# Optimization experiments

Measured on AMD Instinct MI355X. Metric: run time of the kernel, lower is better.

## Reference

```python
import jax, jax.numpy as jnp
import numpy as np

# Fixed hierarchical grouping of the 15 regions into 5 groups of 3 (from split_regions)
SPLIT_IDX = np.array([[0, 1, 8], [2, 4, 6], [3, 5, 7], [9, 11, 13], [10, 12, 14]])
BN_EPS = 1e-5


def _bn_relu(x, g, b):
    # BatchNorm over (batch, spatial) dims in training-stats mode, then ReLU
    mu = jnp.mean(x, axis=(0, 2, 3), keepdims=True)
    var = jnp.var(x, axis=(0, 2, 3), keepdims=True)
    xn = (x - mu) * jax.lax.rsqrt(var + BN_EPS)
    return jax.nn.relu(xn * g[None, :, None, None] + b[None, :, None, None])


def _local_agg(x, params):
    # x: [B, Cin, G, K]; pointwise conv (1x1) -> BN -> ReLU per layer, then max over K
    for W, g, b in params:
        x = jnp.einsum('oi,bigk->bogk', W, x)
        x = _bn_relu(x, g, b)
    return jnp.max(x, axis=-1)  # [B, Cout, G]


def setup_inputs() -> dict:
    key = jax.random.key(0)
    ks = jax.random.split(key, 8)
    B, G, K = 32, 15, 2048
    inp = {"local_regions": jax.random.normal(ks[0], (B, G, K, 3), jnp.float32)}
    chans = [(3, 64, 64), (67, 128, 128), (131, 256, 256)]
    ki = 1
    for li, (c0, c1, c2) in enumerate(chans):
        for wi, (co, ci) in enumerate([(c1, c0), (c2, c1)]):
            inp[f"la{li}_w{wi}"] = jax.random.normal(ks[ki], (co, ci), jnp.float32) * (1.0 / np.sqrt(ci))
            inp[f"la{li}_g{wi}"] = jnp.ones((co,), jnp.float32)
            inp[f"la{li}_b{wi}"] = jnp.zeros((co,), jnp.float32)
            ki += 1
    return inp


def reference(local_regions,
              la0_w0, la0_g0, la0_b0, la0_w1, la0_g1, la0_b1,
              la1_w0, la1_g0, la1_b0, la1_w1, la1_g1, la1_b1,
              la2_w0, la2_g0, la2_b0, la2_w1, la2_g1, la2_b1):
    la0 = [(la0_w0, la0_g0, la0_b0), (la0_w1, la0_g1, la0_b1)]
    la1 = [(la1_w0, la1_g0, la1_b0), (la1_w1, la1_g1, la1_b1)]
    la2 = [(la2_w0, la2_g0, la2_b0), (la2_w1, la2_g1, la2_b1)]
    idx = jnp.asarray(SPLIT_IDX)

    x = jnp.transpose(local_regions, (0, 3, 1, 2))  # [B, 3, 15, K]
    centroids_1 = jnp.mean(x, axis=-1)              # [B, 3, 15]
    relative_1 = x - centroids_1[..., None]
    lf1 = _local_agg(relative_1, la0)               # [B, 64, 15]
    local_features = jnp.concatenate([centroids_1, lf1], axis=1)  # [B, 67, 15]

    # level 2: regroup 15 regions into [5, 3]
    lf1_s = jnp.transpose(lf1, (0, 2, 1))[:, idx, :]         # [B, 5, 3, 64]
    lr2 = jnp.transpose(centroids_1, (0, 2, 1))[:, idx, :]   # [B, 5, 3, 3]
    c2 = jnp.mean(lr2, axis=2)                               # [B, 5, 3]
    rel2 = lr2 - c2[:, :, None, :]
    feats2 = jnp.concatenate([rel2, lf1_s], axis=-1)         # [B, 5, 3, 67]
    feats2 = jnp.transpose(feats2, (0, 3, 1, 2))             # [B, 67, 5, 3]
    lf2 = _local_agg(feats2, la1)                            # [B, 128, 5]

    # level 3: global
    c3 = jnp.mean(c2, axis=1)                                # [B, 3]
    rel3 = c2 - c3[:, None, :]                               # [B, 5, 3]
    lf2 = jnp.concatenate([jnp.transpose(rel3, (0, 2, 1)), lf2], axis=1)  # [B, 131, 5]
    lf2 = lf2[:, :, None, :]                                 # [B, 131, 1, 5]
    gf = _local_agg(lf2, la2)                                # [B, 256, 1]
    return gf.squeeze(2), local_features
```

## Files before the change

### kernel.cpp

```cpp
#include <hip/hip_runtime.h>
#include <math.h>

#define BB 32
#define GG 15
#define KK 2048
#define NB 480
#define N1F 983040.0f
#define EPS 1e-5f
#define PZN ((int)0xAAAAAAAA)

typedef _Float16 half8 __attribute__((ext_vector_type(8)));
typedef float f32x4 __attribute__((ext_vector_type(4)));

#define WS_CENT  0
#define WS_H2B   1920
#define WS_H3B   63360
#define GSREL    104320
#define GBN1     104560
#define G2A      108400
#define G2B      116080
#define G3A      123760
#define G3B      128880
#define FSREL    134000
#define FBN1     134008
#define F2A      134136
#define F2B      134392
#define F3A      134648
#define F3B      135160
#define CNT_GRP  135672
#define CNT_SUP  135864
#define CNT_DONE 135870

#define SMEMF 7936

__device__ const int SIDX[15] = {0,1,8, 2,4,6, 3,5,7, 9,11,13, 10,12,14};
__device__ const int INV[15]  = {0,1,3,6,4,7,5,8,2,9,12,10,13,11,14};

__device__ __forceinline__ float wave_sum(float v){
    for (int off = 32; off; off >>= 1) v += __shfl_down(v, off, 64);
    return v;
}
__device__ __forceinline__ float aloadf(const float* p){
    return __hip_atomic_load(p, __ATOMIC_RELAXED, __HIP_MEMORY_SCOPE_AGENT);
}
__device__ __forceinline__ int aloadi(const int* p){
    return __hip_atomic_load(p, __ATOMIC_RELAXED, __HIP_MEMORY_SCOPE_AGENT);
}
template<int SLP, class Fold>
__device__ __forceinline__ void gbar(int* wsi, int idx, int gi, int ngrp,
                                     int* sflag, Fold fold){
    __syncthreads();
    if (threadIdx.x == 0)
        sflag[0] = (atomicAdd(&wsi[CNT_GRP + idx*32 + gi], 1) == PZN + 15) ? 1 : 0;
    __syncthreads();
    if (sflag[0]) {
        if (threadIdx.x == 0)
            sflag[1] = (atomicAdd(&wsi[CNT_SUP + idx], 1) == PZN + ngrp - 1) ? 1 : 0;
        __syncthreads();
        if (sflag[1]) {
            fold();
            __syncthreads();
            if (threadIdx.x == 0) atomicExch(&wsi[CNT_DONE + idx], 1);
        }
    }
    if (threadIdx.x == 0) {
        int g = 0;
        while (aloadi(&wsi[CNT_DONE + idx]) != 1 && ++g < 4000000)
            __builtin_amdgcn_s_sleep(SLP);
    }
    __syncthreads();
    asm volatile("" ::: "memory");
}

__global__ void __launch_bounds__(256, 2) mega(
        const float* __restrict__ x,
        const float* __restrict__ w00, const float* __restrict__ g00, const float* __restrict__ b00,
        const float* __restrict__ w01, const float* __restrict__ g01, const float* __restrict__ b01,
        const float* __restrict__ w10, const float* __restrict__ g10, const float* __restrict__ b10,
        const float* __restrict__ w11, const float* __restrict__ g11, const float* __restrict__ b11,
        const float* __restrict__ w20, const float* __restrict__ g20, const float* __restrict__ b20,
        const float* __restrict__ w21, const float* __restrict__ g21, const float* __restrict__ b21,
        float* __restrict__ ws, float* __restrict__ out) {
    __shared__ __align__(16) float smemf[SMEMF];
    float* xls  = smemf;
    float* redM = smemf + 6144; float* redN = smemf + 6400;
    float* redS = smemf + 6656; float* redQ = smemf + 6912;
    float* bcast= smemf + 7168;
    float* c2ls = smemf + 7184; float* c3ls = smemf + 7200;
    float* f2ls = smemf + 7204;
    float* vA   = smemf + 7272;
    float* f3ls = smemf + 7400;
    float* h3ls = smemf + 7532;
    int*   sflag= (int*)(smemf + 7916);
    int* wsi = (int*)ws;

    int bid = blockIdx.x, tid = threadIdx.x;
    int b_ = bid / GG, g_ = bid % GG;
    int wv = tid >> 6, lane = tid & 63, l15 = lane & 15, quad = lane >> 4;
    int gi = bid >> 4;

    {
        const float4* xp4 = (const float4*)(x + (size_t)bid * KK * 3);
        float4* xls4 = (float4*)xls;
        #pragma unroll
        for (int i = 0; i < 6; i++) xls4[i*256 + tid] = xp4[i*256 + tid];
        __syncthreads();
        float m[9] = {0,0,0,0,0,0,0,0,0};
        float a[24];
        const float* bp = &xls[tid*24];
        #pragma unroll
        for (int i = 0; i < 6; i++)
            *reinterpret_cast<float4*>(&a[i*4]) = *reinterpret_cast<const float4*>(&bp[i*4]);
        #pragma unroll
        for (int p = 0; p < 8; p++) {
            float ax=a[p*3], ay=a[p*3+1], az=a[p*3+2];
            m[0]+=ax; m[1]+=ay; m[2]+=az;
            m[3]=fmaf(ax,ax,m[3]); m[4]=fmaf(ay,ay,m[4]); m[5]=fmaf(az,az,m[5]);
            m[6]=fmaf(ax,ay,m[6]); m[7]=fmaf(ax,az,m[7]); m[8]=fmaf(ay,az,m[8]);
        }
        #pragma unroll
        for (int q = 0; q < 9; q++) {
            float v = wave_sum(m[q]);
            if (lane == 0) redM[q*4 + wv] = v;
        }
        __syncthreads();
        if (tid == 0) {
            float t[9];
            #pragma unroll
            for (int q = 0; q < 9; q++) t[q] = redM[q*4]+redM[q*4+1]+redM[q*4+2]+redM[q*4+3];
            float c0 = t[0]/KK, c1 = t[1]/KK, c2 = t[2]/KK;
            bcast[0]=c0; bcast[1]=c1; bcast[2]=c2;
            out[8192 + b_*(67*GG) + 0*GG + g_] = c0;
            out[8192 + b_*(67*GG) + 1*GG + g_] = c1;
            out[8192 + b_*(67*GG) + 2*GG + g_] = c2;
            atomicExch(&ws[WS_CENT + bid*4 + 0], c0);
            atomicExch(&ws[WS_CENT + bid*4 + 1], c1);
            atomicExch(&ws[WS_CENT + bid*4 + 2], c2);
            redM[40] = t[3] - KK*c0*c0;  redM[41] = t[4] - KK*c1*c1;
            redM[42] = t[5] - KK*c2*c2;  redM[43] = t[6] - KK*c0*c1;
            redM[44] = t[7] - KK*c0*c2;  redM[45] = t[8] - KK*c1*c2;
        }
        __syncthreads();
    }
    if (tid < 6) atomicAdd(&ws[GSREL + gi*8 + tid], redM[40 + tid]);

    half8 afA[4], afB[4];
    #pragma unroll
    for (int t = 0; t < 4; t++)
        #pragma unroll
        for (int j = 0; j < 8; j++) {
            afA[t][j] = (_Float16)w01[(t*16 + l15)*64 + quad*8 + j];
            afB[t][j] = (_Float16)w01[(t*16 + l15)*64 + 32 + quad*8 + j];
        }
    gbar<8>(wsi, 0, gi, 30, sflag, [&]{
        if (tid < 6) {
            float acc = 0.f;
            #pragma unroll
            for (int s = 0; s < 30; s++) acc += aloadf(&ws[GSREL + s*8 + tid]);
            atomicExch(&ws[FSREL + tid], acc);
        }
    });

    if (tid < 6) bcast[3+tid] = aloadf(&ws[FSREL + tid]) / N1F;
    if (tid >= 64 && tid < 79) {
        int t2 = tid-64, s = t2/3, i = t2%3;
        float acc = 0.f;
        #pragma unroll
        for (int j = 0; j < 3; j++)
            acc += aloadf(&ws[WS_CENT + (b_*GG + SIDX[s*3+j])*4 + i]);
        c2ls[t2] = acc * (1.f/3.f);
    }
    __syncthreads();
    if (tid < 3) {
        float a = 0.f;
        for (int s = 0; s < 5; s++) a += c2ls[s*3+tid];
        c3ls[tid] = a * 0.2f;
    }
    __syncthreads();
    float c0 = bcast[0], c1 = bcast[1], c2v = bcast[2];
    float S00=bcast[3], S11=bcast[4], S22=bcast[5], S01=bcast[6], S02=bcast[7], S12=bcast[8];

    float wa0[8], wa1[8], wa2[8], ba[8], wb0[8], wb1[8], wb2[8], bb[8];
    #pragma unroll
    for (int j = 0; j < 8; j++) {
        int cA = quad*8 + j;
        float u0=w00[cA*3+0], u1=w00[cA*3+1], u2=w00[cA*3+2];
        float var = u0*u0*S00 + u1*u1*S11 + u2*u2*S22
                  + 2.f*(u0*u1*S01 + u0*u2*S02 + u1*u2*S12);
        float a1 = g00[cA]*rsqrtf(var + EPS);
        wa0[j]=a1*u0; wa1[j]=a1*u1; wa2[j]=a1*u2; ba[j]=b00[cA];
        int cB = cA + 32;
        float v0=w00[cB*3+0], v1=w00[cB*3+1], v2=w00[cB*3+2];
        float varB = v0*v0*S00 + v1*v1*S11 + v2*v2*S22
                   + 2.f*(v0*v1*S01 + v0*v2*S02 + v1*v2*S12);
        float a1B = g00[cB]*rsqrtf(varB + EPS);
        wb0[j]=a1B*v0; wb1[j]=a1B*v1; wb2[j]=a1B*v2; bb[j]=b00[cB];
    }
    float mx[16], mn[16], sm[16], sq[16];
    #pragma unroll
    for (int s = 0; s < 16; s++) { mx[s]=-1e30f; mn[s]=1e30f; sm[s]=0.f; sq[s]=0.f; }

    for (int it = 0; it < 32; it++) {
        int k = it*64 + wv*16 + l15;
        float r0 = xls[k*3+0]-c0, r1 = xls[k*3+1]-c1, r2 = xls[k*3+2]-c2v;
        half8 bf0, bf1;
        #pragma unroll
        for (int j = 0; j < 8; j++) {
            float pA = fmaf(wa0[j],r0, fmaf(wa1[j],r1, fmaf(wa2[j],r2, ba[j])));
            bf0[j] = (_Float16)fmaxf(pA, 0.f);
            float pB = fmaf(wb0[j],r0, fmaf(wb1[j],r1, fmaf(wb2[j],r2, bb[j])));
            bf1[j] = (_Float16)fmaxf(pB, 0.f);
        }
        #pragma unroll
        for (int t = 0; t < 4; t++) {
            f32x4 acc = {0.f,0.f,0.f,0.f};
            acc = __builtin_amdgcn_mfma_f32_16x16x32_f16(afA[t], bf0, acc, 0, 0, 0);
            acc = __builtin_amdgcn_mfma_f32_16x16x32_f16(afB[t], bf1, acc, 0, 0, 0);
            #pragma unroll
            for (int r = 0; r < 4; r++) {
                float h = acc[r];
                int s = t*4 + r;
                mx[s]=fmaxf(mx[s],h); mn[s]=fminf(mn[s],h);
                sm[s]+=h;             sq[s]=fmaf(h,h,sq[s]);
            }
        }
    }
    #pragma unroll
    for (int m = 1; m < 16; m <<= 1) {
        #pragma unroll
        for (int s = 0; s < 16; s++) {
            mx[s] = fmaxf(mx[s], __shfl_xor(mx[s], m, 64));
            mn[s] = fminf(mn[s], __shfl_xor(mn[s], m, 64));
            sm[s] += __shfl_xor(sm[s], m, 64);
            sq[s] += __shfl_xor(sq[s], m, 64);
        }
    }
    __syncthreads();
    if (l15 == 0) {
        #pragma unroll
        for (int t = 0; t < 4; t++)
            #pragma unroll
            for (int r = 0; r < 4; r++) {
                int o = t*16 + quad*4 + r;
                redM[wv*64+o]=mx[t*4+r]; redN[wv*64+o]=mn[t*4+r];
                redS[wv*64+o]=sm[t*4+r]; redQ[wv*64+o]=sq[t*4+r];
            }
    }
    __syncthreads();
    float Mreg = -1e30f, Nreg = 1e30f;
    if (tid < 64) {
        float S=0.f, Q=0.f;
        #pragma unroll
        for (int w = 0; w < 4; w++) {
            Mreg = fmaxf(Mreg, redM[w*64+tid]); Nreg = fminf(Nreg, redN[w*64+tid]);
            S += redS[w*64+tid];               Q += redQ[w*64+tid];
        }
        atomicAdd(&ws[GBN1 + gi*128 + tid], S);
        atomicAdd(&ws[GBN1 + gi*128 + 64 + tid], Q);
    }
    gbar<8>(wsi, 1, gi, 30, sflag, [&]{
        if (tid < 128) {
            float acc = 0.f;
            #pragma unroll
            for (int s = 0; s < 30; s++) acc += aloadf(&ws[GBN1 + s*128 + tid]);
            atomicExch(&ws[FBN1 + tid], acc);
        }
    });

    int p_ = INV[g_];

    if (tid < 64) {
        float SM = aloadf(&ws[FBN1 + tid]);
        float SQ = aloadf(&ws[FBN1 + 64 + tid]);
        float mean = SM / N1F;
        float var  = SQ / N1F - mean*mean;
        float s1 = g01[tid]*rsqrtf(var + EPS);
        float t1 = b01[tid] - mean*s1;
        float val = fmaxf(fmaf(s1, (s1 >= 0.f) ? Mreg : Nreg, t1), 0.f);
        f2ls[3+tid] = val;
        out[8192 + b_*(67*GG) + (3+tid)*GG + g_] = val;
    } else if (tid < 67) {
        int i = tid - 64;
        f2ls[i] = bcast[i] - c2ls[(p_/3)*3 + i];
    }
    __syncthreads();

    if (tid < 128) {
        const float* wr = w10 + tid*67;
        float h = 0.f;
        #pragma unroll
        for (int c = 0; c < 67; c++) h = fmaf(wr[c], f2ls[c], h);
        vA[tid] = h;
        atomicAdd(&ws[G2A + gi*256 + tid], h);
        atomicAdd(&ws[G2A + gi*256 + 128 + tid], h*h);
    }
    gbar<4>(wsi, 2, gi, 30, sflag, [&]{
        float acc = 0.f;
        #pragma unroll
        for (int s = 0; s < 30; s++) acc += aloadf(&ws[G2A + s*256 + tid]);
        atomicExch(&ws[F2A + tid], acc);
    });

    {
        int o = tid & 127, ph = tid >> 7;
        if (tid < 128) {
            float mean = aloadf(&ws[F2A + tid]) / 480.f;
            float var  = aloadf(&ws[F2A + 128 + tid]) / 480.f - mean*mean;
            float s2 = g10[tid]*rsqrtf(var+EPS), t2 = b10[tid] - mean*s2;
            vA[tid] = fmaxf(fmaf(s2, vA[tid], t2), 0.f);
        }
        __syncthreads();
        const float* wr = w11 + o*128 + ph*64;
        const float* vv = vA + ph*64;
        float hacc = 0.f;
        #pragma unroll
        for (int j = 0; j < 64; j++) hacc = fmaf(wr[j], vv[j], hacc);
        redM[tid] = hacc;
        __syncthreads();
        if (tid < 128) {
            float h = redM[tid] + redM[tid+128];
            atomicExch(&ws[WS_H2B + (b_*GG + p_)*128 + tid], h);
            atomicAdd(&ws[G2B + gi*256 + tid], h);
            atomicAdd(&ws[G2B + gi*256 + 128 + tid], h*h);
        }
    }
    gbar<4>(wsi, 3, gi, 30, sflag, [&]{
        float acc = 0.f;
        #pragma unroll
        for (int s = 0; s < 30; s++) acc += aloadf(&ws[G2B + s*256 + tid]);
        atomicExch(&ws[F2B + tid], acc);
    });
    if (g_ >= 5) return;

    int pi = b_*5 + g_;
    int gi2 = pi >> 4;

    {
        int s5 = g_;
        if (tid < 128) {
            float mean = aloadf(&ws[F2B + tid]) / 480.f;
            float var  = aloadf(&ws[F2B + 128 + tid]) / 480.f - mean*mean;
            float s3 = g11[tid]*rsqrtf(var+EPS), t3 = b11[tid] - mean*s3;
            float m = -1e30f;
            #pragma unroll
            for (int j = 0; j < 3; j++) {
                float hv = aloadf(&ws[WS_H2B + (b_*GG + s5*3 + j)*128 + tid]);
                m = fmaxf(m, fmaxf(fmaf(s3, hv, t3), 0.f));
            }
            f3ls[3+tid] = m;
        } else if (tid < 131) {
            int i = tid - 128;
            f3ls[i] = c2ls[s5*3+i] - c3ls[i];
        }
        __syncthreads();
        const float* wr = w20 + tid*131;
        float hacc = 0.f;
        #pragma unroll 4
        for (int c = 0; c < 131; c++) hacc = fmaf(wr[c], f3ls[c], hacc);
        h3ls[tid] = hacc;
        atomicAdd(&ws[G3A + gi2*512 + tid], hacc);
        atomicAdd(&ws[G3A + gi2*512 + 256 + tid], hacc*hacc);
    }
    gbar<4>(wsi, 4, gi2, 10, sflag, [&]{
        float a0 = 0.f, a1 = 0.f;
        #pragma unroll
        for (int s = 0; s < 10; s++) {
            a0 += aloadf(&ws[G3A + s*512 + tid]);
            a1 += aloadf(&ws[G3A + s*512 + 256 + tid]);
        }
        atomicExch(&ws[F3A + tid], a0);
        atomicExch(&ws[F3A + 256 + tid], a1);
    });

    {
        float mean = aloadf(&ws[F3A + tid]) / 160.f;
        float var  = aloadf(&ws[F3A + 256 + tid]) / 160.f - mean*mean;
        float s4 = g20[tid]*rsqrtf(var+EPS), t4 = b20[tid] - mean*s4;
        h3ls[tid] = fmaxf(fmaf(s4, h3ls[tid], t4), 0.f);
        __syncthreads();
        const float* wr = w21 + tid*256;
        float hacc = 0.f;
        #pragma unroll 4
        for (int i = 0; i < 256; i++) hacc = fmaf(wr[i], h3ls[i], hacc);
        atomicExch(&ws[WS_H3B + pi*256 + tid], hacc);
        atomicAdd(&ws[G3B + gi2*512 + tid], hacc);
        atomicAdd(&ws[G3B + gi2*512 + 256 + tid], hacc*hacc);
    }
    gbar<4>(wsi, 5, gi2, 10, sflag, [&]{
        float a0 = 0.f, a1 = 0.f;
        #pragma unroll
        for (int s = 0; s < 10; s++) {
            a0 += aloadf(&ws[G3B + s*512 + tid]);
            a1 += aloadf(&ws[G3B + s*512 + 256 + tid]);
        }
        atomicExch(&ws[F3B + tid], a0);
        atomicExch(&ws[F3B + 256 + tid], a1);
    });
    if (g_ != 0) return;

    {
        float SM = aloadf(&ws[F3B + tid]);
        float SQ = aloadf(&ws[F3B + 256 + tid]);
        float mean = SM/160.f, var = SQ/160.f - mean*mean;
        float s5c = g21[tid]*rsqrtf(var+EPS), t5 = b21[tid] - mean*s5c;
        float m = -1e30f;
        #pragma unroll
        for (int jj = 0; jj < 5; jj++) {
            float hv = aloadf(&ws[WS_H3B + (b_*5 + jj)*256 + tid]);
            m = fmaxf(m, fmaxf(fmaf(s5c, hv, t5), 0.f));
        }
        out[b_*256 + tid] = m;
    }
}

extern "C" void kernel_launch(void* const* d_in, const int* in_sizes, int n_in,
                              void* d_out, int out_size, void* d_ws, size_t ws_size,
                              hipStream_t stream) {
    (void)in_sizes; (void)n_in; (void)out_size; (void)ws_size;
    const float* x   = (const float*)d_in[0];
    const float* w00 = (const float*)d_in[1];
    const float* g00 = (const float*)d_in[2];
    const float* b00 = (const float*)d_in[3];
    const float* w01 = (const float*)d_in[4];
    const float* g01 = (const float*)d_in[5];
    const float* b01 = (const float*)d_in[6];
    const float* w10 = (const float*)d_in[7];
    const float* g10 = (const float*)d_in[8];
    const float* b10 = (const float*)d_in[9];
    const float* w11 = (const float*)d_in[10];
    const float* g11 = (const float*)d_in[11];
    const float* b11 = (const float*)d_in[12];
    const float* w20 = (const float*)d_in[13];
    const float* g20 = (const float*)d_in[14];
    const float* b20 = (const float*)d_in[15];
    const float* w21 = (const float*)d_in[16];
    const float* g21 = (const float*)d_in[17];
    const float* b21 = (const float*)d_in[18];
    float* out = (float*)d_out;
    float* ws  = (float*)d_ws;

    mega<<<NB, 256, 0, stream>>>(x, w00,g00,b00, w01,g01,b01, w10,g10,b10,
                                 w11,g11,b11, w20,g20,b20, w21,g21,b21, ws, out);
}
```

Measured before the change: 194.6 us.

## Collapse levels 2-3 onto one block per batch with fewer grid barriers

After level-1 BN stats, each block publishes its per-channel max/min and only the g_=0 block per batch continues. That block builds all 15 level-2 inputs and computes the level-2 and level-3 pointwise layers over multiple points per thread, with register accumulators and local reductions. Grid barriers for the later BN stages now synchronise 32 blocks in 2 groups instead of 480 (or 160) blocks in 30 (or 10) groups, and the per-point workspace round-trips for h2/h3 are removed. The cost is more serial FMA work per surviving block and fewer active blocks during the tail.

```diff
diff --git a/kernel.cpp b/kernel.cpp
--- a/kernel.cpp
+++ b/kernel.cpp
@@ -13,28 +13,26 @@
 typedef float f32x4 __attribute__((ext_vector_type(4)));
 
 #define WS_CENT  0
-#define WS_H2B   1920
-#define WS_H3B   63360
-#define GSREL    104320
-#define GBN1     104560
-#define G2A      108400
-#define G2B      116080
-#define G3A      123760
-#define G3B      128880
-#define FSREL    134000
-#define FBN1     134008
-#define F2A      134136
-#define F2B      134392
-#define F3A      134648
-#define F3B      135160
-#define CNT_GRP  135672
-#define CNT_SUP  135864
-#define CNT_DONE 135870
+#define WS_MN    1920
+#define GSREL    63360
+#define GBN1     63600
+#define G2A      67440
+#define G2B      67952
+#define G3A      68464
+#define G3B      69488
+#define FSREL    70512
+#define FBN1     70520
+#define F2A      70648
+#define F2B      70904
+#define F3A      71160
+#define F3B      71672
+#define CNT_GRP  72184
+#define CNT_SUP  72376
+#define CNT_DONE 72382
 
 #define SMEMF 7936
 
 __device__ const int SIDX[15] = {0,1,8, 2,4,6, 3,5,7, 9,11,13, 10,12,14};
-__device__ const int INV[15]  = {0,1,3,6,4,7,5,8,2,9,12,10,13,11,14};
 
 __device__ __forceinline__ float wave_sum(float v){
     for (int off = 32; off; off >>= 1) v += __shfl_down(v, off, 64);
@@ -86,12 +84,16 @@
     float* redM = smemf + 6144; float* redN = smemf + 6400;
     float* redS = smemf + 6656; float* redQ = smemf + 6912;
     float* bcast= smemf + 7168;
-    float* c2ls = smemf + 7184; float* c3ls = smemf + 7200;
-    float* f2ls = smemf + 7204;
-    float* vA   = smemf + 7272;
-    float* f3ls = smemf + 7400;
-    float* h3ls = smemf + 7532;
     int*   sflag= (int*)(smemf + 7916);
+    float* s1ls  = smemf;
+    float* t1ls  = smemf + 64;
+    float* centls= smemf + 128;
+    float* c2ls  = smemf + 176;
+    float* c3ls  = smemf + 192;
+    float* f2ls  = smemf + 256;
+    float* vls   = smemf + 1280;
+    float* f3ls  = smemf + 3200;
+    float* u3ls  = smemf + 3968;
     int* wsi = (int*)ws;
 
     int bid = blockIdx.x, tid = threadIdx.x;
@@ -162,20 +164,6 @@
     });
 
     if (tid < 6) bcast[3+tid] = aloadf(&ws[FSREL + tid]) / N1F;
-    if (tid >= 64 && tid < 79) {
-        int t2 = tid-64, s = t2/3, i = t2%3;
-        float acc = 0.f;
-        #pragma unroll
-        for (int j = 0; j < 3; j++)
-            acc += aloadf(&ws[WS_CENT + (b_*GG + SIDX[s*3+j])*4 + i]);
-        c2ls[t2] = acc * (1.f/3.f);
-    }
-    __syncthreads();
-    if (tid < 3) {
-        float a = 0.f;
-        for (int s = 0; s < 5; s++) a += c2ls[s*3+tid];
-        c3ls[tid] = a * 0.2f;
-    }
     __syncthreads();
     float c0 = bcast[0], c1 = bcast[1], c2v = bcast[2];
     float S00=bcast[3], S11=bcast[4], S22=bcast[5], S01=bcast[6], S02=bcast[7], S12=bcast[8];
@@ -257,6 +245,8 @@
         }
         atomicAdd(&ws[GBN1 + gi*128 + tid], S);
         atomicAdd(&ws[GBN1 + gi*128 + 64 + tid], Q);
+        atomicExch(&ws[WS_MN + bid*128 + tid], Mreg);
+        atomicExch(&ws[WS_MN + bid*128 + 64 + tid], Nreg);
     }
     gbar<8>(wsi, 1, gi, 30, sflag, [&]{
         if (tid < 128) {
@@ -266,8 +256,6 @@
             atomicExch(&ws[FBN1 + tid], acc);
         }
     });
-
-    int p_ = INV[g_];
 
     if (tid < 64) {
         float SM = aloadf(&ws[FBN1 + tid]);
@@ -277,97 +265,144 @@
         float s1 = g01[tid]*rsqrtf(var + EPS);
         float t1 = b01[tid] - mean*s1;
         float val = fmaxf(fmaf(s1, (s1 >= 0.f) ? Mreg : Nreg, t1), 0.f);
-        f2ls[3+tid] = val;
         out[8192 + b_*(67*GG) + (3+tid)*GG + g_] = val;
-    } else if (tid < 67) {
-        int i = tid - 64;
-        f2ls[i] = bcast[i] - c2ls[(p_/3)*3 + i];
-    }
-    __syncthreads();
-
-    if (tid < 128) {
-        const float* wr = w10 + tid*67;
-        float h = 0.f;
-        #pragma unroll
-        for (int c = 0; c < 67; c++) h = fmaf(wr[c], f2ls[c], h);
-        vA[tid] = h;
-        atomicAdd(&ws[G2A + gi*256 + tid], h);
-        atomicAdd(&ws[G2A + gi*256 + 128 + tid], h*h);
-    }
-    gbar<4>(wsi, 2, gi, 30, sflag, [&]{
-        float acc = 0.f;
-        #pragma unroll
-        for (int s = 0; s < 30; s++) acc += aloadf(&ws[G2A + s*256 + tid]);
-        atomicExch(&ws[F2A + tid], acc);
-    });
-
-    {
-        int o = tid & 127, ph = tid >> 7;
+        s1ls[tid] = s1; t1ls[tid] = t1;
+    }
+    if (g_ != 0) return;
+
+    int git = b_ >> 4;
+    if (tid < 45) centls[tid] = aloadf(&ws[WS_CENT + (b_*GG + tid/3)*4 + tid%3]);
+    __syncthreads();
+    if (tid < 15) {
+        int s = tid/3, i = tid%3;
+        c2ls[tid] = (centls[SIDX[s*3+0]*3+i] + centls[SIDX[s*3+1]*3+i]
+                   + centls[SIDX[s*3+2]*3+i]) * (1.f/3.f);
+    }
+    __syncthreads();
+    if (tid < 3)
+        c3ls[tid] = (c2ls[tid]+c2ls[3+tid]+c2ls[6+tid]+c2ls[9+tid]+c2ls[12+tid]) * 0.2f;
+    if (tid < 45) {
+        int p = tid/3, i = tid%3;
+        f2ls[p*68 + i] = centls[SIDX[p]*3+i] - c2ls[(p/3)*3 + i];
+    }
+    for (int u = tid; u < 960; u += 256) {
+        int p = u >> 6, ch = u & 63, gsrc = SIDX[p];
+        float Mv = aloadf(&ws[WS_MN + (b_*GG + gsrc)*128 + ch]);
+        float Nv = aloadf(&ws[WS_MN + (b_*GG + gsrc)*128 + 64 + ch]);
+        float s1 = s1ls[ch], t1 = t1ls[ch];
+        f2ls[p*68 + 3 + ch] = fmaxf(fmaf(s1, (s1 >= 0.f) ? Mv : Nv, t1), 0.f);
+    }
+    __syncthreads();
+
+    int half = tid >> 7, oc = tid & 127, pbase = half*8, npts = 8 - half;
+    float acc[8];
+    #pragma unroll
+    for (int q = 0; q < 8; q++) acc[q] = 0.f;
+    {
+        const float* wr = w10 + oc*67;
+        #pragma unroll 4
+        for (int c = 0; c < 67; c++) {
+            float wv_ = wr[c];
+            #pragma unroll
+            for (int q = 0; q < 8; q++)
+                acc[q] = fmaf(wv_, f2ls[(pbase+q)*68 + c], acc[q]);
+        }
+        float S = 0.f, Q = 0.f;
+        #pragma unroll
+        for (int q = 0; q < 8; q++) if (q < npts) { S += acc[q]; Q = fmaf(acc[q],acc[q],Q); }
+        redS[tid] = S; redQ[tid] = Q;
+        __syncthreads();
         if (tid < 128) {
-            float mean = aloadf(&ws[F2A + tid]) / 480.f;
-            float var  = aloadf(&ws[F2A + 128 + tid]) / 480.f - mean*mean;
-            float s2 = g10[tid]*rsqrtf(var+EPS), t2 = b10[tid] - mean*s2;
-            vA[tid] = fmaxf(fmaf(s2, vA[tid], t2), 0.f);
-        }
-        __syncthreads();
-        const float* wr = w11 + o*128 + ph*64;
-        const float* vv = vA + ph*64;
-        float hacc = 0.f;
-        #pragma unroll
-        for (int j = 0; j < 64; j++) hacc = fmaf(wr[j], vv[j], hacc);
-        redM[tid] = hacc;
+            atomicAdd(&ws[G2A + git*256 + tid],       redS[tid] + redS[tid+128]);
+            atomicAdd(&ws[G2A + git*256 + 128 + tid], redQ[tid] + redQ[tid+128]);
+        }
+    }
+    gbar<2>(wsi, 2, git, 2, sflag, [&]{
+        float a = aloadf(&ws[G2A + tid]) + aloadf(&ws[G2A + 256 + tid]);
+        atomicExch(&ws[F2A + tid], a);
+    });
+
+    {
+        float mean = aloadf(&ws[F2A + oc]) / 480.f;
+        float var  = aloadf(&ws[F2A + 128 + oc]) / 480.f - mean*mean;
+        float s2 = g10[oc]*rsqrtf(var + EPS), t2 = b10[oc] - mean*s2;
+        #pragma unroll
+        for (int q = 0; q < 8; q++) {
+            float v = fmaxf(fmaf(s2, acc[q], t2), 0.f);
+            if (q < npts) vls[(pbase+q)*128 + oc] = v;
+        }
+    }
+    __syncthreads();
+    #pragma unroll
+    for (int q = 0; q < 8; q++) acc[q] = 0.f;
+    {
+        const float* wr = w11 + oc*128;
+        #pragma unroll 4
+        for (int c = 0; c < 128; c++) {
+            float wv_ = wr[c];
+            #pragma unroll
+            for (int q = 0; q < 8; q++)
+                acc[q] = fmaf(wv_, vls[(pbase+q)*128 + c], acc[q]);
+        }
+        float S = 0.f, Q = 0.f;
+        #pragma unroll
+        for (int q = 0; q < 8; q++) if (q < npts) { S += acc[q]; Q = fmaf(acc[q],acc[q],Q); }
+        redS[tid] = S; redQ[tid] = Q;
         __syncthreads();
         if (tid < 128) {
-            float h = redM[tid] + redM[tid+128];
-            atomicExch(&ws[WS_H2B + (b_*GG + p_)*128 + tid], h);
-            atomicAdd(&ws[G2B + gi*256 + tid], h);
-            atomicAdd(&ws[G2B + gi*256 + 128 + tid], h*h);
-        }
-    }
-    gbar<4>(wsi, 3, gi, 30, sflag, [&]{
-        float acc = 0.f;
-        #pragma unroll
-        for (int s = 0; s < 30; s++) acc += aloadf(&ws[G2B + s*256 + tid]);
-        atomicExch(&ws[F2B + tid], acc);
-    });
-    if (g_ >= 5) return;
-
-    int pi = b_*5 + g_;
-    int gi2 = pi >> 4;
-
-    {
-        int s5 = g_;
-        if (tid < 128) {
-            float mean = aloadf(&ws[F2B + tid]) / 480.f;
-            float var  = aloadf(&ws[F2B + 128 + tid]) / 480.f - mean*mean;
-            float s3 = g11[tid]*rsqrtf(var+EPS), t3 = b11[tid] - mean*s3;
-            float m = -1e30f;
-            #pragma unroll
-            for (int j = 0; j < 3; j++) {
-                float hv = aloadf(&ws[WS_H2B + (b_*GG + s5*3 + j)*128 + tid]);
-                m = fmaxf(m, fmaxf(fmaf(s3, hv, t3), 0.f));
-            }
-            f3ls[3+tid] = m;
-        } else if (tid < 131) {
-            int i = tid - 128;
-            f3ls[i] = c2ls[s5*3+i] - c3ls[i];
-        }
-        __syncthreads();
+            atomicAdd(&ws[G2B + git*256 + tid],       redS[tid] + redS[tid+128]);
+            atomicAdd(&ws[G2B + git*256 + 128 + tid], redQ[tid] + redQ[tid+128]);
+        }
+    }
+    gbar<2>(wsi, 3, git, 2, sflag, [&]{
+        float a = aloadf(&ws[G2B + tid]) + aloadf(&ws[G2B + 256 + tid]);
+        atomicExch(&ws[F2B + tid], a);
+    });
+
+    {
+        float mean = aloadf(&ws[F2B + oc]) / 480.f;
+        float var  = aloadf(&ws[F2B + 128 + oc]) / 480.f - mean*mean;
+        float s3 = g11[oc]*rsqrtf(var + EPS), t3 = b11[oc] - mean*s3;
+        #pragma unroll
+        for (int q = 0; q < 8; q++) {
+            float v = fmaxf(fmaf(s3, acc[q], t3), 0.f);
+            if (q < npts) vls[(pbase+q)*128 + oc] = v;
+        }
+    }
+    __syncthreads();
+    for (int u = tid; u < 640; u += 256) {
+        int s = u >> 7, o2 = u & 127;
+        float m = fmaxf(fmaxf(vls[(3*s)*128+o2], vls[(3*s+1)*128+o2]),
+                        vls[(3*s+2)*128+o2]);
+        f3ls[s*132 + 3 + o2] = m;
+    }
+    if (tid < 15) {
+        int s = tid/3, i = tid%3;
+        f3ls[s*132 + i] = c2ls[tid] - c3ls[i];
+    }
+    __syncthreads();
+
+    float a3[5];
+    #pragma unroll
+    for (int s = 0; s < 5; s++) a3[s] = 0.f;
+    {
         const float* wr = w20 + tid*131;
-        float hacc = 0.f;
         #pragma unroll 4
-        for (int c = 0; c < 131; c++) hacc = fmaf(wr[c], f3ls[c], hacc);
-        h3ls[tid] = hacc;
-        atomicAdd(&ws[G3A + gi2*512 + tid], hacc);
-        atomicAdd(&ws[G3A + gi2*512 + 256 + tid], hacc*hacc);
-    }
-    gbar<4>(wsi, 4, gi2, 10, sflag, [&]{
-        float a0 = 0.f, a1 = 0.f;
-        #pragma unroll
-        for (int s = 0; s < 10; s++) {
-            a0 += aloadf(&ws[G3A + s*512 + tid]);
-            a1 += aloadf(&ws[G3A + s*512 + 256 + tid]);
-        }
+        for (int c = 0; c < 131; c++) {
+            float wv_ = wr[c];
+            #pragma unroll
+            for (int s = 0; s < 5; s++)
+                a3[s] = fmaf(wv_, f3ls[s*132 + c], a3[s]);
+        }
+        float S = 0.f, Q = 0.f;
+        #pragma unroll
+        for (int s = 0; s < 5; s++) { S += a3[s]; Q = fmaf(a3[s],a3[s],Q); }
+        atomicAdd(&ws[G3A + git*512 + tid], S);
+        atomicAdd(&ws[G3A + git*512 + 256 + tid], Q);
+    }
+    gbar<2>(wsi, 4, git, 2, sflag, [&]{
+        float a0 = aloadf(&ws[G3A + tid])       + aloadf(&ws[G3A + 512 + tid]);
+        float a1 = aloadf(&ws[G3A + 256 + tid]) + aloadf(&ws[G3A + 512 + 256 + tid]);
         atomicExch(&ws[F3A + tid], a0);
         atomicExch(&ws[F3A + 256 + tid], a1);
     });
@@ -375,40 +410,44 @@
     {
         float mean = aloadf(&ws[F3A + tid]) / 160.f;
         float var  = aloadf(&ws[F3A + 256 + tid]) / 160.f - mean*mean;
-        float s4 = g20[tid]*rsqrtf(var+EPS), t4 = b20[tid] - mean*s4;
-        h3ls[tid] = fmaxf(fmaf(s4, h3ls[tid], t4), 0.f);
-        __syncthreads();
+        float s4 = g20[tid]*rsqrtf(var + EPS), t4 = b20[tid] - mean*s4;
+        #pragma unroll
+        for (int s = 0; s < 5; s++)
+            u3ls[s*256 + tid] = fmaxf(fmaf(s4, a3[s], t4), 0.f);
+    }
+    __syncthreads();
+    #pragma unroll
+    for (int s = 0; s < 5; s++) a3[s] = 0.f;
+    {
         const float* wr = w21 + tid*256;
-        float hacc = 0.f;
         #pragma unroll 4
-        for (int i = 0; i < 256; i++) hacc = fmaf(wr[i], h3ls[i], hacc);
-        atomicExch(&ws[WS_H3B + pi*256 + tid], hacc);
-        atomicAdd(&ws[G3B + gi2*512 + tid], hacc);
-        atomicAdd(&ws[G3B + gi2*512 + 256 + tid], hacc*hacc);
-    }
-    gbar<4>(wsi, 5, gi2, 10, sflag, [&]{
-        float a0 = 0.f, a1 = 0.f;
-        #pragma unroll
-        for (int s = 0; s < 10; s++) {
-            a0 += aloadf(&ws[G3B + s*512 + tid]);
-            a1 += aloadf(&ws[G3B + s*512 + 256 + tid]);
-        }
+        for (int c = 0; c < 256; c++) {
+            float wv_ = wr[c];
+            #pragma unroll
+            for (int s = 0; s < 5; s++)
+                a3[s] = fmaf(wv_, u3ls[s*256 + c], a3[s]);
+        }
+        float S = 0.f, Q = 0.f;
+        #pragma unroll
+        for (int s = 0; s < 5; s++) { S += a3[s]; Q = fmaf(a3[s],a3[s],Q); }
+        atomicAdd(&ws[G3B + git*512 + tid], S);
+        atomicAdd(&ws[G3B + git*512 + 256 + tid], Q);
+    }
+    gbar<2>(wsi, 5, git, 2, sflag, [&]{
+        float a0 = aloadf(&ws[G3B + tid])       + aloadf(&ws[G3B + 512 + tid]);
+        float a1 = aloadf(&ws[G3B + 256 + tid]) + aloadf(&ws[G3B + 512 + 256 + tid]);
         atomicExch(&ws[F3B + tid], a0);
         atomicExch(&ws[F3B + 256 + tid], a1);
     });
-    if (g_ != 0) return;
-
-    {
-        float SM = aloadf(&ws[F3B + tid]);
-        float SQ = aloadf(&ws[F3B + 256 + tid]);
-        float mean = SM/160.f, var = SQ/160.f - mean*mean;
-        float s5c = g21[tid]*rsqrtf(var+EPS), t5 = b21[tid] - mean*s5c;
+
+    {
+        float mean = aloadf(&ws[F3B + tid]) / 160.f;
+        float var  = aloadf(&ws[F3B + 256 + tid]) / 160.f - mean*mean;
+        float s5 = g21[tid]*rsqrtf(var + EPS), t5 = b21[tid] - mean*s5;
         float m = -1e30f;
         #pragma unroll
-        for (int jj = 0; jj < 5; jj++) {
-            float hv = aloadf(&ws[WS_H3B + (b_*5 + jj)*256 + tid]);
-            m = fmaxf(m, fmaxf(fmaf(s5c, hv, t5), 0.f));
-        }
+        for (int s = 0; s < 5; s++)
+            m = fmaxf(m, fmaxf(fmaf(s5, a3[s], t5), 0.f));
         out[b_*256 + tid] = m;
     }
 }
```

After: 191.1 us. Within noise of the previous version (-1.8%).
